# Kernel optimization log

Hardware: AMD Instinct MI355X
Metric: run time of the kernel (lower is better)

Reference implementation:

```python
import jax, jax.numpy as jnp
import numpy as np

B, N, C = 8, 1025, 768
NUM_HEADS = 12
HEAD_DIM = C // NUM_HEADS  # 64, also depthwise-conv channel count
HW = (32, 32)              # N = 1 + 32*32 (cls token)
SCALE = HEAD_DIM ** -0.5
VALUE_MASK_FILL = -10000.0
LN_EPS = 1e-5


def setup_inputs() -> dict:
    key = jax.random.key(0)
    ks = jax.random.split(key, 12)
    s = 0.02
    inp = {
        "x": jax.random.normal(ks[0], (B, N, C), jnp.float32),
        "mask": jax.random.bernoulli(ks[1], 0.9, (B, N)),
        "Wq": jax.random.normal(ks[2], (C, C), jnp.float32) * s,
        "Wk": jax.random.normal(ks[3], (C, C), jnp.float32) * s,
        "Wv": jax.random.normal(ks[4], (C, C), jnp.float32) * s,
        "pool_q_w": jax.random.normal(ks[5], (HEAD_DIM, 1, 3, 3), jnp.float32) * s,
        "pool_k_w": jax.random.normal(ks[6], (HEAD_DIM, 1, 3, 3), jnp.float32) * s,
        "pool_v_w": jax.random.normal(ks[7], (HEAD_DIM, 1, 3, 3), jnp.float32) * s,
        "gq": jnp.ones((HEAD_DIM,), jnp.float32),
        "bq": jnp.zeros((HEAD_DIM,), jnp.float32),
        "gk": jnp.ones((HEAD_DIM,), jnp.float32),
        "bk": jnp.zeros((HEAD_DIM,), jnp.float32),
        "gv": jnp.ones((HEAD_DIM,), jnp.float32),
        "bv": jnp.zeros((HEAD_DIM,), jnp.float32),
        "Wp": jax.random.normal(ks[8], (C, C), jnp.float32) * s,
        "bp": jnp.zeros((C,), jnp.float32),
    }
    return inp


def _layernorm(t, g, b):
    m = jnp.mean(t, axis=-1, keepdims=True)
    v = jnp.var(t, axis=-1, keepdims=True)
    return (t - m) * jax.lax.rsqrt(v + LN_EPS) * g + b


def _depthwise(t, w):
    # t: [BH, D, H, W], w: [D, 1, 3, 3] depthwise, stride 1, SAME padding
    return jax.lax.conv_general_dilated(
        t, w, window_strides=(1, 1), padding="SAME",
        dimension_numbers=("NCHW", "OIHW", "NCHW"),
        feature_group_count=t.shape[1])


def _attn_pool(t, w, g, b):
    # t: [B, H, N, D] with leading cls token; pool spatial tokens, norm after
    Bb, Hh, Nn, D = t.shape
    cls_tok, spat = t[:, :, :1], t[:, :, 1:]
    Hs, Ws = HW
    spat = spat.reshape(Bb * Hh, Hs, Ws, D).transpose(0, 3, 1, 2)
    spat = _depthwise(spat, w)
    spat = spat.reshape(Bb, Hh, D, Hs * Ws).transpose(0, 1, 3, 2)
    t = jnp.concatenate([cls_tok, spat], axis=2)
    return _layernorm(t, g, b)


def reference(x, mask, Wq, Wk, Wv, pool_q_w, pool_k_w, pool_v_w,
              gq, bq, gk, bk, gv, bv, Wp, bp):
    Bb, Nn, Cc = x.shape
    # QKV projections (no bias), split heads -> [B, H, N, D]
    q = (x @ Wq.T).reshape(Bb, Nn, NUM_HEADS, HEAD_DIM).transpose(0, 2, 1, 3)
    k = (x @ Wk.T).reshape(Bb, Nn, NUM_HEADS, HEAD_DIM).transpose(0, 2, 1, 3)
    v = (x @ Wv.T).reshape(Bb, Nn, NUM_HEADS, HEAD_DIM).transpose(0, 2, 1, 3)
    q = _attn_pool(q, pool_q_w, gq, bq)
    k = _attn_pool(k, pool_k_w, gk, bk)
    v = _attn_pool(v, pool_v_w, gv, bv)
    attn = jnp.einsum("bhqd,bhkd->bhqk", q, k) * SCALE
    # mask: [B, N] bool; broadcast as (B,1,N,1), False -> value_mask_fill
    attn = jnp.where(mask[:, None, :, None], attn, VALUE_MASK_FILL)
    attn = jax.nn.softmax(attn, axis=-1)
    attn_origin = attn
    out = jnp.einsum("bhqk,bhkd->bhqd", attn, v)
    # residual pooling, skipping the cls token
    out = jnp.concatenate([out[:, :, :1], out[:, :, 1:] + q[:, :, 1:]], axis=2)
    out = out.transpose(0, 2, 1, 3).reshape(Bb, Nn, Cc)
    out = out @ Wp.T + bp
    return out, attn_origin
```

## Files before the change

kernel.cpp:

```cpp
#include <hip/hip_runtime.h>
#include <hip/hip_bf16.h>
#include <cstdint>
#include <cstddef>

typedef unsigned short u16;
typedef __attribute__((ext_vector_type(8))) short bf16x8;
typedef __attribute__((ext_vector_type(4))) float f32x4;

#define MFMA16(a,b,c) __builtin_amdgcn_mfma_f32_16x16x32_bf16(a,b,c,0,0,0)
#define GLL16(gp, lp) __builtin_amdgcn_global_load_lds( \
    (const __attribute__((address_space(1))) void*)(gp), \
    (__attribute__((address_space(3))) void*)(lp), 16, 0, 0)

static constexpr int kB = 8, kH = 12, kN = 1025, kC = 768, kD = 64;
static constexpr int kBH = kB*kH;
static constexpr int kNP = 1056;
static constexpr int kM  = kB*kN;
static constexpr float kScale = 0.125f;

__device__ __forceinline__ u16 f2b(float f){
  unsigned u = __builtin_bit_cast(unsigned, f);
  u = (u + 0x7fffu + ((u>>16)&1u)) >> 16;
  return (u16)u;
}
__device__ __forceinline__ float b2f(u16 s){
  unsigned u = ((unsigned)s)<<16;
  return __builtin_bit_cast(float, u);
}
__device__ __forceinline__ unsigned pkbf(float a, float b){
  unsigned r;
  asm("v_cvt_pk_bf16_f32 %0, %1, %2" : "=v"(r) : "v"(a), "v"(b));
  return r;
}
__device__ __forceinline__ int xcd_swz(int orig, int nwg){
  int q = nwg>>3, r = nwg&7;
  int xcd = orig&7, idx = orig>>3;
  return (xcd<r ? xcd*(q+1) : r*(q+1)+(xcd-r)*q) + idx;
}

__global__ __launch_bounds__(256) void k_prep(const float4* __restrict__ x,
    const float* __restrict__ w0, const float* __restrict__ w1,
    const float* __restrict__ w2, const float* __restrict__ w3,
    const unsigned char* __restrict__ m,
    u16* __restrict__ xb, u16* __restrict__ wb, int* __restrict__ maskn){
  __shared__ int cnt;
  const int bid = blockIdx.x;
  if (bid < 6150){
    int i = bid*256 + threadIdx.x;
    float4 v = x[i];
    ushort4 o; o.x=f2b(v.x); o.y=f2b(v.y); o.z=f2b(v.z); o.w=f2b(v.w);
    *reinterpret_cast<ushort4*>(xb + (size_t)i*4) = o;
  } else if (bid < 8454){
    int j = (bid-6150)*256 + threadIdx.x;
    int sel = j/147456, i = j - sel*147456;
    const float* ws[4] = {w0,w1,w2,w3};
    float4 v = reinterpret_cast<const float4*>(ws[sel])[i];
    ushort4 o; o.x=f2b(v.x); o.y=f2b(v.y); o.z=f2b(v.z); o.w=f2b(v.w);
    *reinterpret_cast<ushort4*>(wb + (size_t)sel*589824 + (size_t)i*4) = o;
  } else {
    if (threadIdx.x==0) cnt = 0;
    __syncthreads();
    int local = 0;
    for (int i=threadIdx.x; i<1024; i+=256) local += (m[i]!=0);
    atomicAdd(&cnt, local);
    __syncthreads();
    bool b8 = (cnt > 512);
    int lb = bid - 8454;
    for (int i = lb*256 + threadIdx.x; i < kM; i += 32*256){
      int v = b8 ? (m[i]!=0) : (reinterpret_cast<const int*>(m)[i] != 0);
      maskn[i] = v;
    }
  }
}

template<int MODE>
__global__ __launch_bounds__(256) void k_gemm128(const u16* __restrict__ A,
      const u16* __restrict__ wb, const float* __restrict__ bias,
      u16* __restrict__ outb, float* __restrict__ outf){
  __shared__ union SM {
    struct { u16 a[128*32]; u16 b[128*32]; } s;
    u16 c2[64*136];
  } sm;
  constexpr int NB = (MODE==0) ? 18 : 6;
  const int wg = xcd_swz(blockIdx.x, gridDim.x);
  const int m0 = (wg / NB)*128;
  const int N0 = (wg % NB)*128;
  const int sel = (MODE==0) ? (N0/768) : 3;
  const int jb  = (MODE==0) ? (N0%768) : N0;
  const u16* W = wb + (size_t)sel*589824;
  const int t = threadIdx.x;
  const int wave = t>>6, lane = t&63;
  const int g = lane>>4, cl = lane&15;
  const int wr2 = (wave>>1)*64, wc2 = (wave&1)*64;

  const int cid0 = wave*64 + lane;
  const int cid1 = cid0 + 256;
  const int ar0 = m0 + (cid0>>2) < kM ? m0 + (cid0>>2) : kM-1;
  const int ar1 = m0 + (cid1>>2) < kM ? m0 + (cid1>>2) : kM-1;
  const int ac0 = (cid0&3)<<3, ac1 = (cid1&3)<<3;
  const int br0 = jb + (cid0>>2), br1 = jb + (cid1>>2);
  u16* lA0 = &sm.s.a[(wave*64)*8];
  u16* lA1 = &sm.s.a[(256 + wave*64)*8];
  u16* lB0 = &sm.s.b[(wave*64)*8];
  u16* lB1 = &sm.s.b[(256 + wave*64)*8];

  f32x4 acc[4][4];
  #pragma unroll
  for (int i=0;i<4;i++)
    #pragma unroll
    for (int j=0;j<4;j++) acc[i][j] = (f32x4){0.f,0.f,0.f,0.f};

  for (int k0=0; k0<768; k0+=32){
    __syncthreads();
    GLL16(A + (size_t)ar0*768 + k0 + ac0, lA0);
    GLL16(A + (size_t)ar1*768 + k0 + ac1, lA1);
    GLL16(W + (size_t)br0*768 + k0 + ac0, lB0);
    GLL16(W + (size_t)br1*768 + k0 + ac1, lB1);
    __syncthreads();
    bf16x8 af[4], bfg[4];
    #pragma unroll
    for (int fm=0; fm<4; fm++)
      af[fm] = *reinterpret_cast<const bf16x8*>(&sm.s.a[(wr2+fm*16+cl)*32 + g*8]);
    #pragma unroll
    for (int fn=0; fn<4; fn++)
      bfg[fn] = *reinterpret_cast<const bf16x8*>(&sm.s.b[(wc2+fn*16+cl)*32 + g*8]);
    #pragma unroll
    for (int fm=0; fm<4; fm++)
      #pragma unroll
      for (int fn=0; fn<4; fn++)
        acc[fm][fn] = MFMA16(af[fm], bfg[fn], acc[fm][fn]);
  }

  if (MODE==0){
    #pragma unroll
    for (int ph=0; ph<2; ++ph){
      __syncthreads();
      if ((wave>>1) == ph){
        #pragma unroll
        for (int fm=0; fm<4; fm++)
          #pragma unroll
          for (int fn=0; fn<4; fn++)
            #pragma unroll
            for (int i=0;i<4;i++){
              int r = fm*16 + g*4 + i;
              int c = wc2 + fn*16 + cl;
              sm.c2[r*136 + c] = f2b(acc[fm][fn][i]);
            }
      }
      __syncthreads();
      #pragma unroll
      for (int it=0; it<4; it++){
        int cid = t + it*256;
        int r = cid >> 4, cc = (cid & 15) * 8;
        int gm = m0 + ph*64 + r;
        if (gm < kM){
          *reinterpret_cast<uint4*>(&outb[(size_t)gm*2304 + N0 + cc]) =
              *reinterpret_cast<const uint4*>(&sm.c2[r*136 + cc]);
        }
      }
    }
  } else {
    #pragma unroll
    for (int fm=0; fm<4; fm++)
      #pragma unroll
      for (int fn=0; fn<4; fn++)
        #pragma unroll
        for (int i=0;i<4;i++){
          int gm = m0 + wr2 + fm*16 + g*4 + i;
          if (gm >= kM) continue;
          int gc = jb + wc2 + fn*16 + cl;
          outf[(size_t)gm*768 + gc] = acc[fm][fn][i] + bias[gc];
        }
  }
}

__global__ __launch_bounds__(256) void k_pool3(const u16* __restrict__ qkvmat,
    const float* __restrict__ wq, const float* __restrict__ wk, const float* __restrict__ wv,
    const float* __restrict__ gq, const float* __restrict__ bq,
    const float* __restrict__ gk, const float* __restrict__ bk,
    const float* __restrict__ gv, const float* __restrict__ bv,
    u16* __restrict__ Qp, u16* __restrict__ Kp, u16* __restrict__ Vt){
  __shared__ u16 vt[64][72];
  const int which = blockIdx.y;
  const float* w9 = (which==0)?wq:(which==1)?wk:wv;
  const float* gg = (which==0)?gq:(which==1)?gk:gv;
  const float* bb2= (which==0)?bq:(which==1)?bk:bv;
  u16* out = (which==0)?Qp:(which==1)?Kp:Vt;

  const int wave = threadIdx.x>>6, d = threadIdx.x&63;
  const int wg  = xcd_swz(blockIdx.x, 96*17);
  const int nb  = wg % 17;
  const int bh  = wg / 17;
  const int b = bh/12, h = bh - b*12;
  const int np0 = nb*64;
  const u16* base = qkvmat + ((size_t)b*1025)*2304 + which*768 + h*64;

  float wreg[9];
  #pragma unroll
  for (int j=0;j<9;j++) wreg[j] = w9[d*9+j];
  const float gd = gg[d], bd = bb2[d];

  for (int iter=0; iter<16; ++iter){
    const int np = np0 + iter*4 + wave;
    float v = 0.f;
    if (np < kN){
      if (np == 0){
        v = b2f(base[d]);
      } else {
        int y = (np-1)>>5, x = (np-1)&31;
        #pragma unroll
        for (int ky=0; ky<3; ky++){
          int yy = y+ky-1;
          if (yy<0 || yy>31) continue;
          #pragma unroll
          for (int kx=0; kx<3; kx++){
            int xx = x+kx-1;
            if (xx<0 || xx>31) continue;
            v += wreg[ky*3+kx] * b2f(base[(size_t)(1+yy*32+xx)*2304 + d]);
          }
        }
      }
      float s = v, s2 = v*v;
      #pragma unroll
      for (int off=1; off<64; off<<=1){ s += __shfl_xor(s, off); s2 += __shfl_xor(s2, off); }
      float mean = s*(1.f/64.f);
      float var  = s2*(1.f/64.f) - mean*mean;
      v = (v-mean)*rsqrtf(var+1e-5f)*gd + bd;
    }
    if (which==2) vt[d][iter*4+wave] = f2b(v);
    else if (np < kNP) out[((size_t)bh*kNP + np)*kD + d] = f2b(v);
  }

  if (which==2){
    __syncthreads();
    const int dr = threadIdx.x>>2, seg = threadIdx.x&3;
    if (np0 + seg*16 < kNP){
      u16* dst = Vt + ((size_t)bh*kD + dr)*kNP + np0 + seg*16;
      *reinterpret_cast<uint4*>(dst)     = *reinterpret_cast<const uint4*>(&vt[dr][seg*16]);
      *reinterpret_cast<uint4*>(dst + 8) = *reinterpret_cast<const uint4*>(&vt[dr][seg*16+8]);
    }
  }
}

__global__ __launch_bounds__(512, 8) void k_attn(const u16* __restrict__ Qp, const u16* __restrict__ Kp,
    const u16* __restrict__ Vt, const int* __restrict__ maskn,
    float* __restrict__ attn_out, u16* __restrict__ ctx){
  constexpr int LDE = 1064;
  __shared__ u16 E[16*LDE];
  __shared__ float Lrow[16];
  __shared__ float Linv[16];
  const int wave = threadIdx.x>>6, lane = threadIdx.x&63;
  const int xcd  = blockIdx.x & 7;
  const int slot = blockIdx.x >> 3;
  const int bh = xcd*12 + slot/65;
  const int qt = slot%65;
  const int b  = bh / 12, h = bh - b*12;
  const int qbase = qt*16;
  const int g = lane>>4, cl = lane&15;

  if (threadIdx.x < 16) Lrow[threadIdx.x] = 0.f;
  __syncthreads();

  const u16* qrow = Qp + ((size_t)bh*kNP + (qbase + cl))*kD + g*8;
  bf16x8 aq0 = *reinterpret_cast<const bf16x8*>(qrow);
  bf16x8 aq1 = *reinterpret_cast<const bf16x8*>(qrow + 32);

  const int qi_l = qbase + cl;
  const float mqc = (qi_l < kN && maskn[b*kN + qi_l] != 0) ? kScale : 0.f;

  const u16* kb = Kp + (size_t)bh*kNP*kD;
  float rsum = 0.f;
  u16* erow = &E[cl*LDE];
  #pragma unroll 1
  for (int kt=wave; kt<32; kt+=8){
    const int ktb = kt*32;
    const u16* kr = kb + (size_t)(ktb+cl)*kD + g*8;
    bf16x8 b00 = *reinterpret_cast<const bf16x8*>(kr);
    bf16x8 b01 = *reinterpret_cast<const bf16x8*>(kr+32);
    bf16x8 b10 = *reinterpret_cast<const bf16x8*>(kr+1024);
    bf16x8 b11 = *reinterpret_cast<const bf16x8*>(kr+1024+32);
    f32x4 s0 = {0.f,0.f,0.f,0.f}, s1 = {0.f,0.f,0.f,0.f};
    __builtin_amdgcn_s_setprio(1);
    s0 = MFMA16(b00,aq0,s0); s0 = MFMA16(b01,aq1,s0);
    s1 = MFMA16(b10,aq0,s1); s1 = MFMA16(b11,aq1,s1);
    __builtin_amdgcn_s_setprio(0);
    float e0 = __expf(s0[0]*mqc), e1 = __expf(s0[1]*mqc);
    float e2 = __expf(s0[2]*mqc), e3 = __expf(s0[3]*mqc);
    float f0 = __expf(s1[0]*mqc), f1 = __expf(s1[1]*mqc);
    float f2 = __expf(s1[2]*mqc), f3 = __expf(s1[3]*mqc);
    rsum += ((e0+e1)+(e2+e3)) + ((f0+f1)+(f2+f3));
    uint2 w0v = { pkbf(e0,e1), pkbf(e2,e3) };
    uint2 w1v = { pkbf(f0,f1), pkbf(f2,f3) };
    *reinterpret_cast<uint2*>(&erow[ktb + 4*g])      = w0v;
    *reinterpret_cast<uint2*>(&erow[ktb + 16 + 4*g]) = w1v;
  }
  if (wave == 0){
    const int ktb = 1024;
    const u16* kr = kb + (size_t)(ktb+cl)*kD + g*8;
    bf16x8 b00 = *reinterpret_cast<const bf16x8*>(kr);
    bf16x8 b01 = *reinterpret_cast<const bf16x8*>(kr+32);
    f32x4 s0 = {0.f,0.f,0.f,0.f};
    s0 = MFMA16(b00,aq0,s0); s0 = MFMA16(b01,aq1,s0);
    float e0 = (g==0) ? __expf(s0[0]*mqc) : 0.f;
    rsum += e0;
    uint2 w0v = { pkbf(e0,0.f), 0u };
    uint2 zz  = { 0u, 0u };
    *reinterpret_cast<uint2*>(&erow[ktb + 4*g])      = w0v;
    *reinterpret_cast<uint2*>(&erow[ktb + 16 + 4*g]) = zz;
  }
  rsum += __shfl_xor(rsum, 16);
  rsum += __shfl_xor(rsum, 32);
  if (lane < 16) atomicAdd(&Lrow[cl], rsum);
  __syncthreads();
  if (threadIdx.x < 16) Linv[threadIdx.x] = 1.f/Lrow[threadIdx.x];
  __syncthreads();

  if (wave < 4){
    const int d0 = wave*16;
    f32x4 oacc = (f32x4){0.f,0.f,0.f,0.f};
    const u16* vb = Vt + ((size_t)bh*kD + d0 + cl)*kNP;
    for (int kt=0; kt<33; kt++){
      const int ko = kt*32 + g*8;
      bf16x8 pa = *reinterpret_cast<const bf16x8*>(&E[cl*LDE + ko]);
      bf16x8 vv = *reinterpret_cast<const bf16x8*>(vb + ko);
      oacc = MFMA16(pa, vv, oacc);
    }
    #pragma unroll
    for (int i=0;i<4;i++){
      int row = g*4+i, qi = qbase+row;
      if (qi < kN){
        float val = oacc[i] * Linv[row];
        int dd = d0 + cl;
        if (qi >= 1) val += b2f(Qp[((size_t)bh*kNP + qi)*kD + dd]);
        ctx[((size_t)(b*kN + qi))*kC + h*kD + dd] = f2b(val);
      }
    }
  } else {
    const int t2 = threadIdx.x - 256;
    size_t S = (size_t)bh*kN*kN + (size_t)qbase*kN;
    float* tp = attn_out + S;
    int rows = kN - qbase; if (rows > 16) rows = 16;
    int T = rows*kN;
    int head = (int)((4 - (S & 3)) & 3);
    int body4 = (T - head) >> 2;
    int tail = T - head - body4*4;
    if (t2 < head){
      int e = t2;
      unsigned row = ((unsigned)(e*16369))>>24;
      int col = e - (int)row*kN;
      tp[e] = b2f(E[row*LDE+col]) * Linv[row];
    }
    if (t2 < tail){
      int e = head + body4*4 + t2;
      unsigned row = ((unsigned)(e*16369))>>24;
      int col = e - (int)row*kN;
      tp[e] = b2f(E[row*LDE+col]) * Linv[row];
    }
    for (int idx = t2; idx < body4; idx += 256){
      int e = head + idx*4;
      unsigned row0 = ((unsigned)(e*16369))>>24;
      unsigned row3 = ((unsigned)((e+3)*16369))>>24;
      float4 vv;
      if (row0 == row3){
        int col = e - (int)row0*kN;
        const u16* ep = &E[row0*LDE + col];
        float li = Linv[row0];
        vv.x = b2f(ep[0])*li; vv.y = b2f(ep[1])*li;
        vv.z = b2f(ep[2])*li; vv.w = b2f(ep[3])*li;
      } else {
        float tmp[4];
        #pragma unroll
        for (int j=0;j<4;j++){
          int ee = e+j;
          unsigned row = ((unsigned)(ee*16369))>>24;
          int col = ee - (int)row*kN;
          tmp[j] = b2f(E[row*LDE+col]) * Linv[row];
        }
        vv.x=tmp[0]; vv.y=tmp[1]; vv.z=tmp[2]; vv.w=tmp[3];
      }
      *reinterpret_cast<float4*>(tp + e) = vv;
    }
  }
}

extern "C" void kernel_launch(void* const* d_in, const int* in_sizes, int n_in,
                              void* d_out, int out_size, void* d_ws, size_t ws_size,
                              hipStream_t stream) {
  const float* x    = (const float*)d_in[0];
  const void*  msk  = d_in[1];
  const float* Wq   = (const float*)d_in[2];
  const float* Wk   = (const float*)d_in[3];
  const float* Wv   = (const float*)d_in[4];
  const float* pw_q = (const float*)d_in[5];
  const float* pw_k = (const float*)d_in[6];
  const float* pw_v = (const float*)d_in[7];
  const float* gq   = (const float*)d_in[8];
  const float* bq   = (const float*)d_in[9];
  const float* gk   = (const float*)d_in[10];
  const float* bk   = (const float*)d_in[11];
  const float* gv   = (const float*)d_in[12];
  const float* bv   = (const float*)d_in[13];
  const float* Wp   = (const float*)d_in[14];
  const float* bp   = (const float*)d_in[15];

  char* ws = (char*)d_ws;
  u16* xb     = (u16*)(ws + 0);
  u16* wb     = (u16*)(ws + 12595200);
  int* maskn  = (int*)(ws + 17313792);
  u16* qkvmat = (u16*)(ws + 17346816);
  u16* Qp     = (u16*)(ws + 55132416);
  u16* Kp     = (u16*)(ws + 68108544);
  u16* Vt     = (u16*)(ws + 81084672);
  u16* ctx    = (u16*)(ws + 17346816);

  float* out1 = (float*)d_out;
  float* attn = out1 + (size_t)kM*kC;

  k_prep<<<8486, 256, 0, stream>>>(reinterpret_cast<const float4*>(x),
                                   Wq, Wk, Wv, Wp, (const unsigned char*)msk,
                                   xb, wb, maskn);
  k_gemm128<0><<<65*18, 256, 0, stream>>>(xb, wb, nullptr, qkvmat, nullptr);
  k_pool3<<<dim3(96*17,3), 256, 0, stream>>>(qkvmat, pw_q, pw_k, pw_v,
                                             gq, bq, gk, bk, gv, bv, Qp, Kp, Vt);
  k_attn<<<96*65, 512, 0, stream>>>(Qp, Kp, Vt, maskn, attn, ctx);
  k_gemm128<1><<<65*6, 256, 0, stream>>>(ctx, wb, bp, nullptr, out1);
}
```

Before: 395.9 us.

## Split attention-probability stores into a separate recompute kernel

Result: slower. 525.5 us (+32.7%).

```diff
diff --git a/kernel.cpp b/kernel.cpp
--- a/kernel.cpp
+++ b/kernel.cpp
@@ -244,7 +244,7 @@
 
 __global__ __launch_bounds__(512, 8) void k_attn(const u16* __restrict__ Qp, const u16* __restrict__ Kp,
     const u16* __restrict__ Vt, const int* __restrict__ maskn,
-    float* __restrict__ attn_out, u16* __restrict__ ctx){
+    float* __restrict__ LinvG, u16* __restrict__ ctx){
   constexpr int LDE = 1064;
   __shared__ u16 E[16*LDE];
   __shared__ float Lrow[16];
@@ -335,51 +335,64 @@
         ctx[((size_t)(b*kN + qi))*kC + h*kD + dd] = f2b(val);
       }
     }
-  } else {
-    const int t2 = threadIdx.x - 256;
-    size_t S = (size_t)bh*kN*kN + (size_t)qbase*kN;
-    float* tp = attn_out + S;
-    int rows = kN - qbase; if (rows > 16) rows = 16;
-    int T = rows*kN;
-    int head = (int)((4 - (S & 3)) & 3);
-    int body4 = (T - head) >> 2;
-    int tail = T - head - body4*4;
-    if (t2 < head){
-      int e = t2;
-      unsigned row = ((unsigned)(e*16369))>>24;
-      int col = e - (int)row*kN;
-      tp[e] = b2f(E[row*LDE+col]) * Linv[row];
-    }
-    if (t2 < tail){
-      int e = head + body4*4 + t2;
-      unsigned row = ((unsigned)(e*16369))>>24;
-      int col = e - (int)row*kN;
-      tp[e] = b2f(E[row*LDE+col]) * Linv[row];
-    }
-    for (int idx = t2; idx < body4; idx += 256){
-      int e = head + idx*4;
-      unsigned row0 = ((unsigned)(e*16369))>>24;
-      unsigned row3 = ((unsigned)((e+3)*16369))>>24;
-      float4 vv;
-      if (row0 == row3){
-        int col = e - (int)row0*kN;
-        const u16* ep = &E[row0*LDE + col];
-        float li = Linv[row0];
-        vv.x = b2f(ep[0])*li; vv.y = b2f(ep[1])*li;
-        vv.z = b2f(ep[2])*li; vv.w = b2f(ep[3])*li;
-      } else {
-        float tmp[4];
-        #pragma unroll
-        for (int j=0;j<4;j++){
-          int ee = e+j;
-          unsigned row = ((unsigned)(ee*16369))>>24;
-          int col = ee - (int)row*kN;
-          tmp[j] = b2f(E[row*LDE+col]) * Linv[row];
-        }
-        vv.x=tmp[0]; vv.y=tmp[1]; vv.z=tmp[2]; vv.w=tmp[3];
-      }
-      *reinterpret_cast<float4*>(tp + e) = vv;
-    }
+  } else if (wave == 4){
+    if (lane < 16) LinvG[(size_t)bh*kNP + qbase + lane] = Linv[lane];
+  }
+}
+
+__global__ __launch_bounds__(256) void k_store(const u16* __restrict__ Qp,
+    const u16* __restrict__ Kp, const int* __restrict__ maskn,
+    const float* __restrict__ LinvG, float* __restrict__ attn_out){
+  const int wave = threadIdx.x>>6, lane = threadIdx.x&63;
+  const int xcd  = blockIdx.x & 7;
+  const int slot = blockIdx.x >> 3;
+  const int bh = xcd*12 + slot/65;
+  const int qt = slot%65;
+  const int b  = bh / 12;
+  const int qbase = qt*16;
+  const int g = lane>>4, cl = lane&15;
+
+  const u16* qrow = Qp + ((size_t)bh*kNP + (qbase + cl))*kD + g*8;
+  bf16x8 aq0 = *reinterpret_cast<const bf16x8*>(qrow);
+  bf16x8 aq1 = *reinterpret_cast<const bf16x8*>(qrow + 32);
+
+  const int qi_l = qbase + cl;
+  const bool rowok = qi_l < kN;
+  const float mqc = (rowok && maskn[b*kN + qi_l] != 0) ? kScale : 0.f;
+  const float linv = LinvG[(size_t)bh*kNP + qi_l];
+
+  const u16* kb = Kp + (size_t)bh*kNP*kD;
+  float* arow = attn_out + (size_t)bh*kN*kN + (size_t)qi_l*kN;
+
+  #pragma unroll 2
+  for (int kt=wave; kt<32; kt+=4){
+    const int ktb = kt*32;
+    const u16* kr = kb + (size_t)(ktb+cl)*kD + g*8;
+    bf16x8 b00 = *reinterpret_cast<const bf16x8*>(kr);
+    bf16x8 b01 = *reinterpret_cast<const bf16x8*>(kr+32);
+    bf16x8 b10 = *reinterpret_cast<const bf16x8*>(kr+1024);
+    bf16x8 b11 = *reinterpret_cast<const bf16x8*>(kr+1024+32);
+    f32x4 s0 = {0.f,0.f,0.f,0.f}, s1 = {0.f,0.f,0.f,0.f};
+    s0 = MFMA16(b00,aq0,s0); s0 = MFMA16(b01,aq1,s0);
+    s1 = MFMA16(b10,aq0,s1); s1 = MFMA16(b11,aq1,s1);
+    f32x4 p0, p1;
+    #pragma unroll
+    for (int j=0;j<4;j++){
+      p0[j] = __expf(s0[j]*mqc)*linv;
+      p1[j] = __expf(s1[j]*mqc)*linv;
+    }
+    if (rowok){
+      *reinterpret_cast<f32x4*>(arow + ktb + 4*g)      = p0;
+      *reinterpret_cast<f32x4*>(arow + ktb + 16 + 4*g) = p1;
+    }
+  }
+  if (wave == 0){
+    const u16* kr = kb + (size_t)(1024+cl)*kD + g*8;
+    bf16x8 b00 = *reinterpret_cast<const bf16x8*>(kr);
+    bf16x8 b01 = *reinterpret_cast<const bf16x8*>(kr+32);
+    f32x4 s0 = {0.f,0.f,0.f,0.f};
+    s0 = MFMA16(b00,aq0,s0); s0 = MFMA16(b01,aq1,s0);
+    if (rowok && g == 0) arow[1024] = __expf(s0[0]*mqc)*linv;
   }
 }
 
@@ -408,10 +421,11 @@
   u16* wb     = (u16*)(ws + 12595200);
   int* maskn  = (int*)(ws + 17313792);
   u16* qkvmat = (u16*)(ws + 17346816);
+  u16* ctx    = (u16*)(ws + 17346816);
+  float* LinvG= (float*)(ws + 29942016);
   u16* Qp     = (u16*)(ws + 55132416);
   u16* Kp     = (u16*)(ws + 68108544);
   u16* Vt     = (u16*)(ws + 81084672);
-  u16* ctx    = (u16*)(ws + 17346816);
 
   float* out1 = (float*)d_out;
   float* attn = out1 + (size_t)kM*kC;
@@ -422,6 +436,7 @@
   k_gemm128<0><<<65*18, 256, 0, stream>>>(xb, wb, nullptr, qkvmat, nullptr);
   k_pool3<<<dim3(96*17,3), 256, 0, stream>>>(qkvmat, pw_q, pw_k, pw_v,
                                              gq, bq, gk, bk, gv, bv, Qp, Kp, Vt);
-  k_attn<<<96*65, 512, 0, stream>>>(Qp, Kp, Vt, maskn, attn, ctx);
+  k_attn<<<96*65, 512, 0, stream>>>(Qp, Kp, Vt, maskn, LinvG, ctx);
+  k_store<<<96*65, 256, 0, stream>>>(Qp, Kp, maskn, LinvG, attn);
   k_gemm128<1><<<65*6, 256, 0, stream>>>(ctx, wb, bp, nullptr, out1);
 }
```

## Process 32 query rows per attention block and split attn writeback across waves

Applied to the files above, without the earlier changes.

Result: no change. 389.7 us, median of 2 (-1.6%).

```diff
diff --git a/kernel.cpp b/kernel.cpp
--- a/kernel.cpp
+++ b/kernel.cpp
@@ -31,6 +31,9 @@
   unsigned r;
   asm("v_cvt_pk_bf16_f32 %0, %1, %2" : "=v"(r) : "v"(a), "v"(b));
   return r;
+}
+__device__ __forceinline__ unsigned div1025(unsigned e){
+  return (unsigned)(((unsigned long long)e * 65473ull) >> 26);
 }
 __device__ __forceinline__ int xcd_swz(int orig, int nwg){
   int q = nwg>>3, r = nwg&7;
@@ -242,35 +245,39 @@
   }
 }
 
-__global__ __launch_bounds__(512, 8) void k_attn(const u16* __restrict__ Qp, const u16* __restrict__ Kp,
+__global__ __launch_bounds__(512, 4) void k_attn(const u16* __restrict__ Qp, const u16* __restrict__ Kp,
     const u16* __restrict__ Vt, const int* __restrict__ maskn,
     float* __restrict__ attn_out, u16* __restrict__ ctx){
   constexpr int LDE = 1064;
-  __shared__ u16 E[16*LDE];
-  __shared__ float Lrow[16];
-  __shared__ float Linv[16];
+  __shared__ u16 E[32*LDE];
+  __shared__ float Lrow[32];
+  __shared__ float Linv[32];
   const int wave = threadIdx.x>>6, lane = threadIdx.x&63;
   const int xcd  = blockIdx.x & 7;
   const int slot = blockIdx.x >> 3;
-  const int bh = xcd*12 + slot/65;
-  const int qt = slot%65;
+  const int bh = xcd*12 + slot/33;
+  const int qt = slot%33;
   const int b  = bh / 12, h = bh - b*12;
-  const int qbase = qt*16;
+  const int qbase = qt*32;
   const int g = lane>>4, cl = lane&15;
 
-  if (threadIdx.x < 16) Lrow[threadIdx.x] = 0.f;
+  if (threadIdx.x < 32) Lrow[threadIdx.x] = 0.f;
   __syncthreads();
 
-  const u16* qrow = Qp + ((size_t)bh*kNP + (qbase + cl))*kD + g*8;
-  bf16x8 aq0 = *reinterpret_cast<const bf16x8*>(qrow);
-  bf16x8 aq1 = *reinterpret_cast<const bf16x8*>(qrow + 32);
-
-  const int qi_l = qbase + cl;
-  const float mqc = (qi_l < kN && maskn[b*kN + qi_l] != 0) ? kScale : 0.f;
+  const u16* qrow0 = Qp + ((size_t)bh*kNP + (qbase + cl))*kD + g*8;
+  bf16x8 aq0 = *reinterpret_cast<const bf16x8*>(qrow0);
+  bf16x8 aq1 = *reinterpret_cast<const bf16x8*>(qrow0 + 32);
+  bf16x8 aq2 = *reinterpret_cast<const bf16x8*>(qrow0 + 16*kD);
+  bf16x8 aq3 = *reinterpret_cast<const bf16x8*>(qrow0 + 16*kD + 32);
+
+  const int qi0 = qbase + cl, qi1 = qbase + 16 + cl;
+  const float mq0 = (qi0 < kN && maskn[b*kN + qi0] != 0) ? kScale : 0.f;
+  const float mq1 = (qi1 < kN && maskn[b*kN + qi1] != 0) ? kScale : 0.f;
 
   const u16* kb = Kp + (size_t)bh*kNP*kD;
-  float rsum = 0.f;
-  u16* erow = &E[cl*LDE];
+  float rs0 = 0.f, rs1 = 0.f;
+  u16* erow0 = &E[cl*LDE];
+  u16* erow1 = &E[(16+cl)*LDE];
   #pragma unroll 1
   for (int kt=wave; kt<32; kt+=8){
     const int ktb = kt*32;
@@ -280,86 +287,84 @@
     bf16x8 b10 = *reinterpret_cast<const bf16x8*>(kr+1024);
     bf16x8 b11 = *reinterpret_cast<const bf16x8*>(kr+1024+32);
     f32x4 s0 = {0.f,0.f,0.f,0.f}, s1 = {0.f,0.f,0.f,0.f};
+    f32x4 s2 = {0.f,0.f,0.f,0.f}, s3 = {0.f,0.f,0.f,0.f};
     __builtin_amdgcn_s_setprio(1);
     s0 = MFMA16(b00,aq0,s0); s0 = MFMA16(b01,aq1,s0);
     s1 = MFMA16(b10,aq0,s1); s1 = MFMA16(b11,aq1,s1);
+    s2 = MFMA16(b00,aq2,s2); s2 = MFMA16(b01,aq3,s2);
+    s3 = MFMA16(b10,aq2,s3); s3 = MFMA16(b11,aq3,s3);
     __builtin_amdgcn_s_setprio(0);
-    float e0 = __expf(s0[0]*mqc), e1 = __expf(s0[1]*mqc);
-    float e2 = __expf(s0[2]*mqc), e3 = __expf(s0[3]*mqc);
-    float f0 = __expf(s1[0]*mqc), f1 = __expf(s1[1]*mqc);
-    float f2 = __expf(s1[2]*mqc), f3 = __expf(s1[3]*mqc);
-    rsum += ((e0+e1)+(e2+e3)) + ((f0+f1)+(f2+f3));
+    float e0=__expf(s0[0]*mq0), e1=__expf(s0[1]*mq0), e2=__expf(s0[2]*mq0), e3=__expf(s0[3]*mq0);
+    float f0=__expf(s1[0]*mq0), f1=__expf(s1[1]*mq0), f2=__expf(s1[2]*mq0), f3=__expf(s1[3]*mq0);
+    float g0=__expf(s2[0]*mq1), g1=__expf(s2[1]*mq1), g2=__expf(s2[2]*mq1), g3=__expf(s2[3]*mq1);
+    float h0=__expf(s3[0]*mq1), h1=__expf(s3[1]*mq1), h2=__expf(s3[2]*mq1), h3=__expf(s3[3]*mq1);
+    rs0 += ((e0+e1)+(e2+e3)) + ((f0+f1)+(f2+f3));
+    rs1 += ((g0+g1)+(g2+g3)) + ((h0+h1)+(h2+h3));
     uint2 w0v = { pkbf(e0,e1), pkbf(e2,e3) };
     uint2 w1v = { pkbf(f0,f1), pkbf(f2,f3) };
-    *reinterpret_cast<uint2*>(&erow[ktb + 4*g])      = w0v;
-    *reinterpret_cast<uint2*>(&erow[ktb + 16 + 4*g]) = w1v;
+    uint2 w2v = { pkbf(g0,g1), pkbf(g2,g3) };
+    uint2 w3v = { pkbf(h0,h1), pkbf(h2,h3) };
+    *reinterpret_cast<uint2*>(&erow0[ktb + 4*g])      = w0v;
+    *reinterpret_cast<uint2*>(&erow0[ktb + 16 + 4*g]) = w1v;
+    *reinterpret_cast<uint2*>(&erow1[ktb + 4*g])      = w2v;
+    *reinterpret_cast<uint2*>(&erow1[ktb + 16 + 4*g]) = w3v;
   }
   if (wave == 0){
     const int ktb = 1024;
     const u16* kr = kb + (size_t)(ktb+cl)*kD + g*8;
     bf16x8 b00 = *reinterpret_cast<const bf16x8*>(kr);
     bf16x8 b01 = *reinterpret_cast<const bf16x8*>(kr+32);
-    f32x4 s0 = {0.f,0.f,0.f,0.f};
+    f32x4 s0 = {0.f,0.f,0.f,0.f}, s2 = {0.f,0.f,0.f,0.f};
     s0 = MFMA16(b00,aq0,s0); s0 = MFMA16(b01,aq1,s0);
-    float e0 = (g==0) ? __expf(s0[0]*mqc) : 0.f;
-    rsum += e0;
+    s2 = MFMA16(b00,aq2,s2); s2 = MFMA16(b01,aq3,s2);
+    float e0 = (g==0) ? __expf(s0[0]*mq0) : 0.f;
+    float g0 = (g==0) ? __expf(s2[0]*mq1) : 0.f;
+    rs0 += e0; rs1 += g0;
     uint2 w0v = { pkbf(e0,0.f), 0u };
+    uint2 w2v = { pkbf(g0,0.f), 0u };
     uint2 zz  = { 0u, 0u };
-    *reinterpret_cast<uint2*>(&erow[ktb + 4*g])      = w0v;
-    *reinterpret_cast<uint2*>(&erow[ktb + 16 + 4*g]) = zz;
-  }
-  rsum += __shfl_xor(rsum, 16);
-  rsum += __shfl_xor(rsum, 32);
-  if (lane < 16) atomicAdd(&Lrow[cl], rsum);
+    *reinterpret_cast<uint2*>(&erow0[ktb + 4*g])      = w0v;
+    *reinterpret_cast<uint2*>(&erow0[ktb + 16 + 4*g]) = zz;
+    *reinterpret_cast<uint2*>(&erow1[ktb + 4*g])      = w2v;
+    *reinterpret_cast<uint2*>(&erow1[ktb + 16 + 4*g]) = zz;
+  }
+  rs0 += __shfl_xor(rs0, 16);  rs0 += __shfl_xor(rs0, 32);
+  rs1 += __shfl_xor(rs1, 16);  rs1 += __shfl_xor(rs1, 32);
+  if (lane < 16){
+    atomicAdd(&Lrow[cl], rs0);
+    atomicAdd(&Lrow[16+cl], rs1);
+  }
   __syncthreads();
-  if (threadIdx.x < 16) Linv[threadIdx.x] = 1.f/Lrow[threadIdx.x];
+  if (threadIdx.x < 32) Linv[threadIdx.x] = 1.f/Lrow[threadIdx.x];
   __syncthreads();
 
-  if (wave < 4){
-    const int d0 = wave*16;
-    f32x4 oacc = (f32x4){0.f,0.f,0.f,0.f};
-    const u16* vb = Vt + ((size_t)bh*kD + d0 + cl)*kNP;
-    for (int kt=0; kt<33; kt++){
-      const int ko = kt*32 + g*8;
-      bf16x8 pa = *reinterpret_cast<const bf16x8*>(&E[cl*LDE + ko]);
-      bf16x8 vv = *reinterpret_cast<const bf16x8*>(vb + ko);
-      oacc = MFMA16(pa, vv, oacc);
-    }
-    #pragma unroll
-    for (int i=0;i<4;i++){
-      int row = g*4+i, qi = qbase+row;
-      if (qi < kN){
-        float val = oacc[i] * Linv[row];
-        int dd = d0 + cl;
-        if (qi >= 1) val += b2f(Qp[((size_t)bh*kNP + qi)*kD + dd]);
-        ctx[((size_t)(b*kN + qi))*kC + h*kD + dd] = f2b(val);
-      }
-    }
-  } else {
+  size_t S = (size_t)bh*kN*kN + (size_t)qbase*kN;
+  float* tp = attn_out + S;
+  int rows = kN - qbase; if (rows > 32) rows = 32;
+  int T = rows*kN;
+  int head = (int)((4 - (S & 3)) & 3);
+  int body4 = (T - head) >> 2;
+  int tail = T - head - body4*4;
+  int B1 = (body4*5) >> 3;
+
+  if (wave >= 4){
     const int t2 = threadIdx.x - 256;
-    size_t S = (size_t)bh*kN*kN + (size_t)qbase*kN;
-    float* tp = attn_out + S;
-    int rows = kN - qbase; if (rows > 16) rows = 16;
-    int T = rows*kN;
-    int head = (int)((4 - (S & 3)) & 3);
-    int body4 = (T - head) >> 2;
-    int tail = T - head - body4*4;
     if (t2 < head){
       int e = t2;
-      unsigned row = ((unsigned)(e*16369))>>24;
+      unsigned row = div1025((unsigned)e);
       int col = e - (int)row*kN;
       tp[e] = b2f(E[row*LDE+col]) * Linv[row];
     }
     if (t2 < tail){
       int e = head + body4*4 + t2;
-      unsigned row = ((unsigned)(e*16369))>>24;
+      unsigned row = div1025((unsigned)e);
       int col = e - (int)row*kN;
       tp[e] = b2f(E[row*LDE+col]) * Linv[row];
     }
-    for (int idx = t2; idx < body4; idx += 256){
+    for (int idx = t2; idx < B1; idx += 256){
       int e = head + idx*4;
-      unsigned row0 = ((unsigned)(e*16369))>>24;
-      unsigned row3 = ((unsigned)((e+3)*16369))>>24;
+      unsigned row0 = div1025((unsigned)e);
+      unsigned row3 = div1025((unsigned)(e+3));
       float4 vv;
       if (row0 == row3){
         int col = e - (int)row0*kN;
@@ -372,7 +377,60 @@
         #pragma unroll
         for (int j=0;j<4;j++){
           int ee = e+j;
-          unsigned row = ((unsigned)(ee*16369))>>24;
+          unsigned row = div1025((unsigned)ee);
+          int col = ee - (int)row*kN;
+          tmp[j] = b2f(E[row*LDE+col]) * Linv[row];
+        }
+        vv.x=tmp[0]; vv.y=tmp[1]; vv.z=tmp[2]; vv.w=tmp[3];
+      }
+      *reinterpret_cast<float4*>(tp + e) = vv;
+    }
+  } else {
+    const int d0 = wave*16;
+    f32x4 oa0 = (f32x4){0.f,0.f,0.f,0.f};
+    f32x4 oa1 = (f32x4){0.f,0.f,0.f,0.f};
+    const u16* vb = Vt + ((size_t)bh*kD + d0 + cl)*kNP;
+    for (int kt=0; kt<33; kt++){
+      const int ko = kt*32 + g*8;
+      bf16x8 vv = *reinterpret_cast<const bf16x8*>(vb + ko);
+      bf16x8 pa0 = *reinterpret_cast<const bf16x8*>(&E[cl*LDE + ko]);
+      bf16x8 pa1 = *reinterpret_cast<const bf16x8*>(&E[(16+cl)*LDE + ko]);
+      oa0 = MFMA16(pa0, vv, oa0);
+      oa1 = MFMA16(pa1, vv, oa1);
+    }
+    #pragma unroll
+    for (int i=0;i<4;i++){
+      int row = g*4+i, qi = qbase+row;
+      int dd = d0 + cl;
+      if (qi < kN){
+        float val = oa0[i] * Linv[row];
+        if (qi >= 1) val += b2f(Qp[((size_t)bh*kNP + qi)*kD + dd]);
+        ctx[((size_t)(b*kN + qi))*kC + h*kD + dd] = f2b(val);
+      }
+      int row1 = 16 + g*4 + i, qi1b = qbase + row1;
+      if (qi1b < kN){
+        float val = oa1[i] * Linv[row1];
+        if (qi1b >= 1) val += b2f(Qp[((size_t)bh*kNP + qi1b)*kD + dd]);
+        ctx[((size_t)(b*kN + qi1b))*kC + h*kD + dd] = f2b(val);
+      }
+    }
+    for (int idx = B1 + threadIdx.x; idx < body4; idx += 256){
+      int e = head + idx*4;
+      unsigned row0 = div1025((unsigned)e);
+      unsigned row3 = div1025((unsigned)(e+3));
+      float4 vv;
+      if (row0 == row3){
+        int col = e - (int)row0*kN;
+        const u16* ep = &E[row0*LDE + col];
+        float li = Linv[row0];
+        vv.x = b2f(ep[0])*li; vv.y = b2f(ep[1])*li;
+        vv.z = b2f(ep[2])*li; vv.w = b2f(ep[3])*li;
+      } else {
+        float tmp[4];
+        #pragma unroll
+        for (int j=0;j<4;j++){
+          int ee = e+j;
+          unsigned row = div1025((unsigned)ee);
           int col = ee - (int)row*kN;
           tmp[j] = b2f(E[row*LDE+col]) * Linv[row];
         }
@@ -422,6 +480,6 @@
   k_gemm128<0><<<65*18, 256, 0, stream>>>(xb, wb, nullptr, qkvmat, nullptr);
   k_pool3<<<dim3(96*17,3), 256, 0, stream>>>(qkvmat, pw_q, pw_k, pw_v,
                                              gq, bq, gk, bk, gv, bv, Qp, Kp, Vt);
-  k_attn<<<96*65, 512, 0, stream>>>(Qp, Kp, Vt, maskn, attn, ctx);
+  k_attn<<<96*33, 512, 0, stream>>>(Qp, Kp, Vt, maskn, attn, ctx);
   k_gemm128<1><<<65*6, 256, 0, stream>>>(ctx, wb, bp, nullptr, out1);
 }
```
